# Performance work log

Hardware: AMD Instinct MI355X
Metric: run time of the kernel (lower is better)

Reference implementation:

```python
import jax, jax.numpy as jnp
import numpy as np

D_MODEL, N_HEADS, N_GROUPS, BASE = 2048, 32, 8, 10000
HEAD_DIM = D_MODEL // N_HEADS  # 64


def _rope_cache(seq, head_dim, base=BASE):
    half = head_dim // 2
    theta = 1.0 / (base ** (jnp.arange(0, head_dim, 2)[:half].astype(jnp.float32) / head_dim))
    ang = jnp.einsum('i,j->ij', jnp.arange(seq, dtype=jnp.float32), theta)  # (seq, half)
    return jnp.cos(ang), jnp.sin(ang)


def _apply_rope(x):
    # x: (b, s, h, head_dim) -> interleaved-pair rotation, matching torch module
    b, s, h, hd = x.shape
    cos, sin = _rope_cache(s, hd)
    xr = x.reshape(b, s, h, hd // 2, 2)
    c = cos[None, :, None, :]
    sn = sin[None, :, None, :]
    x0, x1 = xr[..., 0], xr[..., 1]
    out = jnp.stack((x0 * c - x1 * sn, x1 * c + x0 * sn), axis=-1)
    return out.reshape(b, s, h, hd).astype(x.dtype)


def setup_inputs() -> dict:
    key = jax.random.key(0)
    ks = jax.random.split(key, 8)
    B, S = 1, 2048
    kv_dim = HEAD_DIM * N_GROUPS
    return {
        'Q': jax.random.normal(ks[0], (B, S, D_MODEL), jnp.float32),
        'K': jax.random.normal(ks[1], (B, S, D_MODEL), jnp.float32),
        'V': jax.random.normal(ks[2], (B, S, D_MODEL), jnp.float32),
        'attention_mask': jnp.ones((B, S), jnp.int32),
        'Wq': jax.random.normal(ks[3], (D_MODEL, D_MODEL), jnp.float32) * 0.02,
        'Wk': jax.random.normal(ks[4], (D_MODEL, kv_dim), jnp.float32) * 0.02,
        'Wv': jax.random.normal(ks[5], (D_MODEL, kv_dim), jnp.float32) * 0.02,
        'Wo': jax.random.normal(ks[6], (D_MODEL, D_MODEL), jnp.float32) * 0.02,
        'bo': jnp.zeros((D_MODEL,), jnp.float32),
    }


def reference(Q, K, V, attention_mask, Wq, Wk, Wv, Wo, bo):
    b, s, _ = Q.shape
    g, hpg, hd = N_GROUPS, N_HEADS // N_GROUPS, HEAD_DIM
    # projections (weights stored as [in, out], equivalent to torch x @ W.T)
    q = (Q @ Wq).reshape(b, s, N_HEADS, hd)
    q = _apply_rope(q).reshape(b, s, g, hpg, hd)
    k = _apply_rope((K @ Wk).reshape(b, s, g, hd))
    v = (V @ Wv).reshape(b, s, g, hd)

    scale = jnp.sqrt(jnp.float32(hd))
    scores = jnp.einsum('bnghd,bmgd->bnghm', q, k) / scale  # (b, s, g, hpg, s)
    # padding mask (b, 1, 1, 1, s) and causal mask (1, s, 1, 1, s)
    pad = (attention_mask != 0)[:, None, None, None, :]
    causal = jnp.tril(jnp.ones((s, s), bool))[None, :, None, None, :]
    scores = jnp.where(pad & causal, scores, -jnp.inf)
    attn = jax.nn.softmax(scores, axis=-1)  # dropout p=0.0 -> identity
    out = jnp.einsum('bnghm,bmgd->bnghd', attn, v).reshape(b, s, D_MODEL)
    return out @ Wo + bo
```

## Files before the change

### kernel.cpp

```cpp
#include <hip/hip_runtime.h>

typedef __bf16 bf16_t;
typedef __bf16 bf16x8 __attribute__((ext_vector_type(8)));
typedef __bf16 bf16x4 __attribute__((ext_vector_type(4)));
typedef __bf16 bf16x2 __attribute__((ext_vector_type(2)));
typedef float  f32x4  __attribute__((ext_vector_type(4)));

#define LOG2E 1.44269504088896340736f

#define GLDS(gp, lp)                                                           \
  __builtin_amdgcn_global_load_lds(                                            \
      (const __attribute__((address_space(1))) void*)(gp),                     \
      (__attribute__((address_space(3))) void*)(lp), 16, 0, 0)

__global__ __launch_bounds__(256) void rope_table_k(float* __restrict__ cs,
                                                    float* __restrict__ sn, int S) {
  int i = blockIdx.x * 256 + threadIdx.x;
  if (i >= S * 32) return;
  int s = i >> 5, j = i & 31;
  float theta = powf(10000.0f, -(float)j * (1.0f / 32.0f));
  float a = (float)s * theta;
  cs[i] = cosf(a);
  sn[i] = sinf(a);
}

__global__ void transpose4_k(const float* __restrict__ Wq, const float* __restrict__ Wk,
                             const float* __restrict__ Wv, const float* __restrict__ Wo,
                             bf16_t* __restrict__ WqT, bf16_t* __restrict__ WkT,
                             bf16_t* __restrict__ WvT, bf16_t* __restrict__ WoT) {
  __shared__ float tile[32][33];
  const int bx = blockIdx.x;
  const float* in; bf16_t* out; int C, cbl;
  if (bx < 64)      { in = Wq; out = WqT; C = 2048; cbl = bx; }
  else if (bx < 80) { in = Wk; out = WkT; C = 512;  cbl = bx - 64; }
  else if (bx < 96) { in = Wv; out = WvT; C = 512;  cbl = bx - 80; }
  else              { in = Wo; out = WoT; C = 2048; cbl = bx - 96; }
  const int R = 2048;
  int c0 = cbl * 32, r0 = blockIdx.y * 32;
  int tx = threadIdx.x, ty = threadIdx.y;
  #pragma unroll
  for (int k = 0; k < 32; k += 8)
    tile[ty + k][tx] = in[(size_t)(r0 + ty + k) * C + c0 + tx];
  __syncthreads();
  #pragma unroll
  for (int k = 0; k < 32; k += 8)
    out[(size_t)(c0 + ty + k) * R + r0 + tx] = (bf16_t)tile[tx][ty + k];
}

__device__ __forceinline__ int xcd_swz(int bid, int nb) {
  const int q = nb >> 3;
  return (bid & 7) * q + (bid >> 3);
}
__device__ __forceinline__ void st_map(int lin, int nstc, int& rb, int& cb) {
  const int stid = lin >> 4, w = lin & 15;
  const int sr = stid / nstc, t = stid - sr * nstc;
  const int sc = (sr & 1) ? (nstc - 1 - t) : t;
  rb = sr * 4 + (w >> 2);
  cb = sc * 4 + (w & 3);
}

template<int MODE>
__global__ __launch_bounds__(256) void gemm_glds_k(
    const void* __restrict__ Aq, const void* __restrict__ Ak, const void* __restrict__ Av,
    const bf16_t* __restrict__ Bq, const bf16_t* __restrict__ Bk, const bf16_t* __restrict__ Bv,
    const int K, const float* __restrict__ cs, const float* __restrict__ sn,
    bf16_t* __restrict__ oq, bf16_t* __restrict__ okg, bf16_t* __restrict__ ovt,
    float* __restrict__ ofp, const float* __restrict__ bias, const int S) {
  constexpr int BN   = (MODE == 0) ? 128 : 64;
  constexpr int NI   = BN / 32;
  constexpr int BU   = BN / 32;
  constexpr int NB   = (MODE == 0) ? 768 : 1024;
  constexpr int NSTC = (MODE == 0) ? 6 : 8;
  __shared__ bf16_t a_lds[64 * 64];
  __shared__ bf16_t b_lds[BN * 64];
  const int tid = threadIdx.x, wid = tid >> 6, lane = tid & 63;
  const int fr = lane & 15, kg = lane >> 4;

  const int lin = xcd_swz(blockIdx.x, NB);
  int rb, cb; st_map(lin, NSTC, rb, cb);
  const void* Ap; const bf16_t* Bp; int emode, col0;
  if (MODE == 1)    { Ap = Aq; Bp = Bq; emode = 3; col0 = cb * BN; }
  else if (cb < 16) { Ap = Aq; Bp = Bq; emode = 0; col0 = cb * 128; }
  else if (cb < 20) { Ap = Ak; Bp = Bk; emode = 1; col0 = (cb - 16) * 128; }
  else              { Ap = Av; Bp = Bv; emode = 2; col0 = (cb - 20) * 128; }
  const int row0 = rb * 64;
  const int wr = (wid >> 1) * 32, wc = (wid & 1) * (BN / 2);

  f32x4 acc[2][NI];
  #pragma unroll
  for (int i = 0; i < 2; ++i)
    #pragma unroll
    for (int j = 0; j < NI; ++j)
      acc[i][j] = (f32x4){0.f, 0.f, 0.f, 0.f};

  const int rloc = lane >> 3;
  const int schunk = ((lane & 7) ^ rloc) * 8;
  const bf16_t* gB[BU];
  bf16_t* lB[BU];
  #pragma unroll
  for (int u = 0; u < BU; ++u) {
    gB[u] = Bp + (size_t)(col0 + (wid * BU + u) * 8 + rloc) * K + schunk;
    lB[u] = &b_lds[(wid * BU + u) * 512];
  }

#define MFMA_STEP                                                              \
  do {                                                                         \
    _Pragma("unroll")                                                          \
    for (int ks = 0; ks < 2; ++ks) {                                           \
      bf16x8 af[2], bfr[NI];                                                   \
      _Pragma("unroll")                                                        \
      for (int mi = 0; mi < 2; ++mi) {                                         \
        const int r = wr + mi * 16 + fr;                                       \
        af[mi] = *(const bf16x8*)&a_lds[r * 64 + (((ks * 4 + kg) ^ (fr & 7)) * 8)]; \
      }                                                                        \
      _Pragma("unroll")                                                        \
      for (int ni = 0; ni < NI; ++ni) {                                        \
        const int r = wc + ni * 16 + fr;                                       \
        bfr[ni] = *(const bf16x8*)&b_lds[r * 64 + (((ks * 4 + kg) ^ (fr & 7)) * 8)]; \
      }                                                                        \
      _Pragma("unroll")                                                        \
      for (int mi = 0; mi < 2; ++mi)                                           \
        _Pragma("unroll")                                                      \
        for (int ni = 0; ni < NI; ++ni)                                        \
          acc[mi][ni] = __builtin_amdgcn_mfma_f32_16x16x32_bf16(af[mi], bfr[ni], acc[mi][ni], 0, 0, 0); \
    }                                                                          \
  } while (0)

  if (MODE == 0) {
    const float* Afp = (const float*)Ap;
    const int arow = wid * 16 + (lane >> 2);
    const int acol = (lane & 3) * 16;
    const int c0w = (lane & 3) * 2;
    const int wofs0 = arow * 64 + ((c0w ^ (arow & 7)) * 8);
    const int wofs1 = arow * 64 + (((c0w + 1) ^ (arow & 7)) * 8);
    const float* abase = &Afp[(size_t)(row0 + arow) * K + acol];
    f32x4 pA0, pA1, pA2, pA3, pB0, pB1, pB2, pB3;
    pA0 = *(const f32x4*)(abase);      pA1 = *(const f32x4*)(abase + 4);
    pA2 = *(const f32x4*)(abase + 8);  pA3 = *(const f32x4*)(abase + 12);
    pB0 = *(const f32x4*)(abase + 64); pB1 = *(const f32x4*)(abase + 68);
    pB2 = *(const f32x4*)(abase + 72); pB3 = *(const f32x4*)(abase + 76);

#define A_WRITE(r0_, r1_, r2_, r3_)                                            \
    do {                                                                       \
      bf16x8 w0, w1;                                                           \
      w0[0]=(bf16_t)r0_[0]; w0[1]=(bf16_t)r0_[1]; w0[2]=(bf16_t)r0_[2]; w0[3]=(bf16_t)r0_[3]; \
      w0[4]=(bf16_t)r1_[0]; w0[5]=(bf16_t)r1_[1]; w0[6]=(bf16_t)r1_[2]; w0[7]=(bf16_t)r1_[3]; \
      w1[0]=(bf16_t)r2_[0]; w1[1]=(bf16_t)r2_[1]; w1[2]=(bf16_t)r2_[2]; w1[3]=(bf16_t)r2_[3]; \
      w1[4]=(bf16_t)r3_[0]; w1[5]=(bf16_t)r3_[1]; w1[6]=(bf16_t)r3_[2]; w1[7]=(bf16_t)r3_[3]; \
      *(bf16x8*)&a_lds[wofs0] = w0;                                            \
      *(bf16x8*)&a_lds[wofs1] = w1;                                            \
    } while (0)

    for (int kt = 0; kt < K; kt += 128) {
      __syncthreads();
      A_WRITE(pA0, pA1, pA2, pA3);
      #pragma unroll
      for (int u = 0; u < BU; ++u) GLDS(gB[u] + kt, lB[u]);
      __syncthreads();
      if (kt + 128 < K) {
        const float* p = abase + kt + 128;
        pA0 = *(const f32x4*)(p);     pA1 = *(const f32x4*)(p + 4);
        pA2 = *(const f32x4*)(p + 8); pA3 = *(const f32x4*)(p + 12);
      }
      MFMA_STEP;
      __syncthreads();
      A_WRITE(pB0, pB1, pB2, pB3);
      #pragma unroll
      for (int u = 0; u < BU; ++u) GLDS(gB[u] + kt + 64, lB[u]);
      __syncthreads();
      if (kt + 192 < K) {
        const float* p = abase + kt + 192;
        pB0 = *(const f32x4*)(p);     pB1 = *(const f32x4*)(p + 4);
        pB2 = *(const f32x4*)(p + 8); pB3 = *(const f32x4*)(p + 12);
      }
      MFMA_STEP;
    }
#undef A_WRITE
  } else {
    const bf16_t* gA0 = (const bf16_t*)Ap + (size_t)(row0 + (wid * 2 + 0) * 8 + rloc) * K + schunk;
    const bf16_t* gA1 = (const bf16_t*)Ap + (size_t)(row0 + (wid * 2 + 1) * 8 + rloc) * K + schunk;
    bf16_t* lA0 = &a_lds[(wid * 2 + 0) * 512];
    bf16_t* lA1 = &a_lds[(wid * 2 + 1) * 512];
    for (int kt = 0; kt < K; kt += 64) {
      __syncthreads();
      GLDS(gA0 + kt, lA0);
      GLDS(gA1 + kt, lA1);
      #pragma unroll
      for (int u = 0; u < BU; ++u) GLDS(gB[u] + kt, lB[u]);
      __syncthreads();
      MFMA_STEP;
    }
  }
#undef MFMA_STEP

  #pragma unroll
  for (int mi = 0; mi < 2; ++mi) {
    #pragma unroll
    for (int ni = 0; ni < NI; ++ni) {
      #pragma unroll
      for (int r = 0; r < 4; ++r) {
        const int grow = row0 + wr + mi * 16 + kg * 4 + r;
        const int gcol = col0 + wc + ni * 16 + fr;
        float v = acc[mi][ni][r];
        if (emode == 3) {
          ofp[(size_t)grow * 2048 + gcol] = v + bias[gcol];
        } else if (emode == 2) {
          const int gi = gcol >> 6, d = gcol & 63;
          ovt[((size_t)gi * 64 + d) * S + grow] = (bf16_t)v;
        } else {
          const float pv = __shfl_xor(v, 1);
          const int d = gcol & 63, p = d >> 1, hh = gcol >> 6;
          const float c = cs[grow * 32 + p], s = sn[grow * 32 + p];
          float o = (d & 1) ? fmaf(pv, s, v * c) : fmaf(-pv, s, v * c);
          if (emode == 0) {
            o *= 0.125f * LOG2E;
            oq[((size_t)hh * S + grow) * 64 + d] = (bf16_t)o;
          } else {
            okg[((size_t)hh * S + grow) * 64 + d] = (bf16_t)o;
          }
        }
      }
    }
  }
}

__device__ __forceinline__ int swz8(int r, int c) { return r * 64 + (((c) ^ (r & 7)) << 3); }

__global__ __launch_bounds__(256) void attn_k(
    const bf16_t* __restrict__ qh,
    const bf16_t* __restrict__ kgr,
    const bf16_t* __restrict__ vtg,
    const int* __restrict__ amask,
    bf16_t* __restrict__ ao,
    const int S) {
  __shared__ bf16_t k_lds[64 * 64];
  __shared__ bf16_t vt_lds[64 * 64];
  __shared__ bf16_t p_lds[4][16 * 64];
  const int tid = threadIdx.x, wid = tid >> 6, lane = tid & 63;
  const int fr = lane & 15, kgp = lane >> 4;
  const int h = blockIdx.x, g = h >> 2;
  const int qb = 31 - blockIdx.y;
  const int q0 = qb * 64 + wid * 16;
  const int qg = q0 + fr;

  const bf16_t* qbase = qh + ((size_t)h * S + q0 + fr) * 64;
  const bf16x8 qf0 = *(const bf16x8*)&qbase[kgp * 8];
  const bf16x8 qf1 = *(const bf16x8*)&qbase[32 + kgp * 8];

  f32x4 oacc[4];
  #pragma unroll
  for (int t = 0; t < 4; ++t) oacc[t] = (f32x4){0.f, 0.f, 0.f, 0.f};
  float m_ = -1e30f, l_ = 0.f;

  const int srow = tid >> 2, sc4 = tid & 3;
  const bf16_t* kbase = kgr + (size_t)g * S * 64;
  const bf16_t* vbase = vtg + (size_t)g * 64 * S;
  const int cmax = qb + 1;

  bf16x8 nk0 = *(const bf16x8*)&kbase[(size_t)srow * 64 + sc4 * 8];
  bf16x8 nk1 = *(const bf16x8*)&kbase[(size_t)srow * 64 + 32 + sc4 * 8];
  bf16x8 nv0 = *(const bf16x8*)&vbase[(size_t)srow * S + sc4 * 8];
  bf16x8 nv1 = *(const bf16x8*)&vbase[(size_t)srow * S + 32 + sc4 * 8];
  int mvc = amask[lane];
  *(bf16x8*)&k_lds[swz8(srow, sc4)]      = nk0;
  *(bf16x8*)&k_lds[swz8(srow, 4 + sc4)]  = nk1;
  *(bf16x8*)&vt_lds[swz8(srow, sc4)]     = nv0;
  *(bf16x8*)&vt_lds[swz8(srow, 4 + sc4)] = nv1;
  __syncthreads();

  for (int c = 0; c < cmax; ++c) {
    const int kc0 = c * 64;
    const unsigned long long pm = __ballot(mvc == 0);
    const bool more = (c + 1 < cmax);
    if (more) {
      const int kc1 = kc0 + 64;
      nk0 = *(const bf16x8*)&kbase[(size_t)(kc1 + srow) * 64 + sc4 * 8];
      nk1 = *(const bf16x8*)&kbase[(size_t)(kc1 + srow) * 64 + 32 + sc4 * 8];
      nv0 = *(const bf16x8*)&vbase[(size_t)srow * S + kc1 + sc4 * 8];
      nv1 = *(const bf16x8*)&vbase[(size_t)srow * S + kc1 + 32 + sc4 * 8];
      mvc = amask[kc1 + lane];
    }

    f32x4 sc[4];
    #pragma unroll
    for (int a = 0; a < 4; ++a) {
      const bf16x8 ka0 = *(const bf16x8*)&k_lds[swz8(a * 16 + fr, kgp)];
      const bf16x8 ka1 = *(const bf16x8*)&k_lds[swz8(a * 16 + fr, 4 + kgp)];
      f32x4 z = (f32x4){0.f, 0.f, 0.f, 0.f};
      z = __builtin_amdgcn_mfma_f32_16x16x32_bf16(ka0, qf0, z, 0, 0, 0);
      z = __builtin_amdgcn_mfma_f32_16x16x32_bf16(ka1, qf1, z, 0, 0, 0);
      sc[a] = z;
    }

    if (c == qb) {
      #pragma unroll
      for (int a = 0; a < 4; ++a)
        #pragma unroll
        for (int r = 0; r < 4; ++r) {
          const int kl = a * 16 + 4 * kgp + r;
          if (kc0 + kl > qg) sc[a][r] = -1e30f;
        }
    }
    if (pm) {
      #pragma unroll
      for (int a = 0; a < 4; ++a)
        #pragma unroll
        for (int r = 0; r < 4; ++r) {
          const int kl = a * 16 + 4 * kgp + r;
          if ((pm >> kl) & 1) sc[a][r] = -1e30f;
        }
    }

    float t0 = fmaxf(fmaxf(sc[0][0], sc[0][1]), fmaxf(sc[0][2], sc[0][3]));
    float t1 = fmaxf(fmaxf(sc[1][0], sc[1][1]), fmaxf(sc[1][2], sc[1][3]));
    float t2 = fmaxf(fmaxf(sc[2][0], sc[2][1]), fmaxf(sc[2][2], sc[2][3]));
    float t3 = fmaxf(fmaxf(sc[3][0], sc[3][1]), fmaxf(sc[3][2], sc[3][3]));
    float smax = fmaxf(fmaxf(t0, t1), fmaxf(t2, t3));
    smax = fmaxf(smax, __shfl_xor(smax, 16));
    smax = fmaxf(smax, __shfl_xor(smax, 32));

    const bool rescale = !__all(smax <= m_ + 8.0f);
    if (rescale) {
      const float mn = fmaxf(m_, smax);
      const float al = exp2f(m_ - mn);
      m_ = mn;
      #pragma unroll
      for (int t = 0; t < 4; ++t)
        #pragma unroll
        for (int r = 0; r < 4; ++r) oacc[t][r] *= al;
      l_ *= al;
    }

    float ps = 0.f;
    #pragma unroll
    for (int a = 0; a < 4; ++a)
      #pragma unroll
      for (int r = 0; r < 4; ++r) {
        const float p = exp2f(sc[a][r] - m_);
        sc[a][r] = p;
        ps += p;
      }
    ps += __shfl_xor(ps, 16);
    ps += __shfl_xor(ps, 32);
    l_ += ps;

    #pragma unroll
    for (int a = 0; a < 4; ++a) {
      bf16x4 w;
      w[0] = (bf16_t)sc[a][0];
      w[1] = (bf16_t)sc[a][1];
      w[2] = (bf16_t)sc[a][2];
      w[3] = (bf16_t)sc[a][3];
      const int off = a * 16 + 4 * kgp;
      *(bf16x4*)&p_lds[wid][fr * 64 + (((off >> 3) ^ (fr & 7)) << 3) + (off & 7)] = w;
    }
    const bf16x8 pa0 = *(const bf16x8*)&p_lds[wid][swz8(fr, kgp)];
    const bf16x8 pa1 = *(const bf16x8*)&p_lds[wid][swz8(fr, 4 + kgp)];

    #pragma unroll
    for (int t = 0; t < 4; ++t) {
      const bf16x8 vb0 = *(const bf16x8*)&vt_lds[swz8(t * 16 + fr, kgp)];
      const bf16x8 vb1 = *(const bf16x8*)&vt_lds[swz8(t * 16 + fr, 4 + kgp)];
      oacc[t] = __builtin_amdgcn_mfma_f32_16x16x32_bf16(vb0, pa0, oacc[t], 0, 0, 0);
      oacc[t] = __builtin_amdgcn_mfma_f32_16x16x32_bf16(vb1, pa1, oacc[t], 0, 0, 0);
    }

    if (more) {
      __syncthreads();
      *(bf16x8*)&k_lds[swz8(srow, sc4)]      = nk0;
      *(bf16x8*)&k_lds[swz8(srow, 4 + sc4)]  = nk1;
      *(bf16x8*)&vt_lds[swz8(srow, sc4)]     = nv0;
      *(bf16x8*)&vt_lds[swz8(srow, 4 + sc4)] = nv1;
      __syncthreads();
    }
  }

  const float inv = 1.0f / l_;
  #pragma unroll
  for (int t = 0; t < 4; ++t) {
    bf16x4 o4;
    #pragma unroll
    for (int r = 0; r < 4; ++r) o4[r] = (bf16_t)(oacc[t][r] * inv);
    *(bf16x4*)&ao[(size_t)(q0 + fr) * 2048 + h * 64 + t * 16 + 4 * kgp] = o4;
  }
}

extern "C" void kernel_launch(void* const* d_in, const int* in_sizes, int n_in,
                              void* d_out, int out_size, void* d_ws, size_t ws_size,
                              hipStream_t stream) {
  const float* Q  = (const float*)d_in[0];
  const float* K  = (const float*)d_in[1];
  const float* V  = (const float*)d_in[2];
  const int*   am = (const int*)d_in[3];
  const float* Wq = (const float*)d_in[4];
  const float* Wk = (const float*)d_in[5];
  const float* Wv = (const float*)d_in[6];
  const float* Wo = (const float*)d_in[7];
  const float* bo = (const float*)d_in[8];
  float* out = (float*)d_out;

  const int S = 2048, D = 2048;
  char* w = (char*)d_ws;
  const size_t MB = 1u << 20;
  bf16_t* WqT = (bf16_t*)(w + 0 * MB);
  bf16_t* WoT = (bf16_t*)(w + 8 * MB);
  bf16_t* WkT = (bf16_t*)(w + 16 * MB);
  bf16_t* WvT = (bf16_t*)(w + 18 * MB);
  bf16_t* qh  = (bf16_t*)(w + 20 * MB);
  bf16_t* kgr = (bf16_t*)(w + 28 * MB);
  bf16_t* vtg = (bf16_t*)(w + 30 * MB);
  bf16_t* ao  = (bf16_t*)(w + 32 * MB);
  float*  cs  = (float*)(w + 40 * MB);
  float*  sn  = (float*)(w + 40 * MB + 256 * 1024);

  rope_table_k<<<256, 256, 0, stream>>>(cs, sn, S);
  transpose4_k<<<dim3(160, 64), dim3(32, 8), 0, stream>>>(Wq, Wk, Wv, Wo, WqT, WkT, WvT, WoT);

  gemm_glds_k<0><<<768, 256, 0, stream>>>(Q, K, V, WqT, WkT, WvT, D,
                                          cs, sn, qh, kgr, vtg, nullptr, nullptr, S);

  attn_k<<<dim3(32, 32), 256, 0, stream>>>(qh, kgr, vtg, am, ao, S);

  gemm_glds_k<1><<<1024, 256, 0, stream>>>(ao, nullptr, nullptr, WoT, nullptr, nullptr,
                                           D, nullptr, nullptr, nullptr, nullptr, nullptr,
                                           out, bo, S);
}
```

Before: 142.0 us.

## Double-buffer LDS tiles in projection GEMMs to overlap loads with MFMA

Gives the A and B shared-memory tiles two buffers in both GEMM modes. Each iteration stages the next K-slice into the alternate buffer while MFMAs run on the current one, with a single barrier per iteration instead of two. This is meant to hide global-to-LDS latency and cut synchronization stalls. The cost is twice the LDS per block, which may lower occupancy.

Measured after the change: 147.3 us. +3.7%, slower.

```diff
diff --git a/kernel.cpp b/kernel.cpp
--- a/kernel.cpp
+++ b/kernel.cpp
@@ -71,8 +71,8 @@
   constexpr int BU   = BN / 32;
   constexpr int NB   = (MODE == 0) ? 768 : 1024;
   constexpr int NSTC = (MODE == 0) ? 6 : 8;
-  __shared__ bf16_t a_lds[64 * 64];
-  __shared__ bf16_t b_lds[BN * 64];
+  __shared__ bf16_t a_lds[2][64 * 64];
+  __shared__ bf16_t b_lds[2][BN * 64];
   const int tid = threadIdx.x, wid = tid >> 6, lane = tid & 63;
   const int fr = lane & 15, kg = lane >> 4;
 
@@ -96,14 +96,18 @@
   const int rloc = lane >> 3;
   const int schunk = ((lane & 7) ^ rloc) * 8;
   const bf16_t* gB[BU];
-  bf16_t* lB[BU];
-  #pragma unroll
-  for (int u = 0; u < BU; ++u) {
+  #pragma unroll
+  for (int u = 0; u < BU; ++u)
     gB[u] = Bp + (size_t)(col0 + (wid * BU + u) * 8 + rloc) * K + schunk;
-    lB[u] = &b_lds[(wid * BU + u) * 512];
-  }
-
-#define MFMA_STEP                                                              \
+  const int lBo = (wid * BU) * 512;
+
+#define STAGE_B(buf, kt)                                                       \
+  do {                                                                         \
+    _Pragma("unroll")                                                          \
+    for (int u = 0; u < BU; ++u) GLDS(gB[u] + (kt), &b_lds[buf][lBo + u * 512]); \
+  } while (0)
+
+#define MFMA_STEP(buf)                                                         \
   do {                                                                         \
     _Pragma("unroll")                                                          \
     for (int ks = 0; ks < 2; ++ks) {                                           \
@@ -111,12 +115,12 @@
       _Pragma("unroll")                                                        \
       for (int mi = 0; mi < 2; ++mi) {                                         \
         const int r = wr + mi * 16 + fr;                                       \
-        af[mi] = *(const bf16x8*)&a_lds[r * 64 + (((ks * 4 + kg) ^ (fr & 7)) * 8)]; \
+        af[mi] = *(const bf16x8*)&a_lds[buf][r * 64 + (((ks * 4 + kg) ^ (fr & 7)) * 8)]; \
       }                                                                        \
       _Pragma("unroll")                                                        \
       for (int ni = 0; ni < NI; ++ni) {                                        \
         const int r = wc + ni * 16 + fr;                                       \
-        bfr[ni] = *(const bf16x8*)&b_lds[r * 64 + (((ks * 4 + kg) ^ (fr & 7)) * 8)]; \
+        bfr[ni] = *(const bf16x8*)&b_lds[buf][r * 64 + (((ks * 4 + kg) ^ (fr & 7)) * 8)]; \
       }                                                                        \
       _Pragma("unroll")                                                        \
       for (int mi = 0; mi < 2; ++mi)                                           \
@@ -134,64 +138,74 @@
     const int wofs0 = arow * 64 + ((c0w ^ (arow & 7)) * 8);
     const int wofs1 = arow * 64 + (((c0w + 1) ^ (arow & 7)) * 8);
     const float* abase = &Afp[(size_t)(row0 + arow) * K + acol];
-    f32x4 pA0, pA1, pA2, pA3, pB0, pB1, pB2, pB3;
-    pA0 = *(const f32x4*)(abase);      pA1 = *(const f32x4*)(abase + 4);
-    pA2 = *(const f32x4*)(abase + 8);  pA3 = *(const f32x4*)(abase + 12);
-    pB0 = *(const f32x4*)(abase + 64); pB1 = *(const f32x4*)(abase + 68);
-    pB2 = *(const f32x4*)(abase + 72); pB3 = *(const f32x4*)(abase + 76);
-
-#define A_WRITE(r0_, r1_, r2_, r3_)                                            \
+    f32x4 r0_, r1_, r2_, r3_;
+
+#define LOAD_A(off)                                                            \
+    do {                                                                       \
+      const float* p = abase + (off);                                          \
+      r0_ = *(const f32x4*)(p);     r1_ = *(const f32x4*)(p + 4);              \
+      r2_ = *(const f32x4*)(p + 8); r3_ = *(const f32x4*)(p + 12);             \
+    } while (0)
+#define A_WRITE(buf)                                                           \
     do {                                                                       \
       bf16x8 w0, w1;                                                           \
       w0[0]=(bf16_t)r0_[0]; w0[1]=(bf16_t)r0_[1]; w0[2]=(bf16_t)r0_[2]; w0[3]=(bf16_t)r0_[3]; \
       w0[4]=(bf16_t)r1_[0]; w0[5]=(bf16_t)r1_[1]; w0[6]=(bf16_t)r1_[2]; w0[7]=(bf16_t)r1_[3]; \
       w1[0]=(bf16_t)r2_[0]; w1[1]=(bf16_t)r2_[1]; w1[2]=(bf16_t)r2_[2]; w1[3]=(bf16_t)r2_[3]; \
       w1[4]=(bf16_t)r3_[0]; w1[5]=(bf16_t)r3_[1]; w1[6]=(bf16_t)r3_[2]; w1[7]=(bf16_t)r3_[3]; \
-      *(bf16x8*)&a_lds[wofs0] = w0;                                            \
-      *(bf16x8*)&a_lds[wofs1] = w1;                                            \
+      *(bf16x8*)&a_lds[buf][wofs0] = w0;                                       \
+      *(bf16x8*)&a_lds[buf][wofs1] = w1;                                       \
     } while (0)
 
-    for (int kt = 0; kt < K; kt += 128) {
-      __syncthreads();
-      A_WRITE(pA0, pA1, pA2, pA3);
-      #pragma unroll
-      for (int u = 0; u < BU; ++u) GLDS(gB[u] + kt, lB[u]);
-      __syncthreads();
-      if (kt + 128 < K) {
-        const float* p = abase + kt + 128;
-        pA0 = *(const f32x4*)(p);     pA1 = *(const f32x4*)(p + 4);
-        pA2 = *(const f32x4*)(p + 8); pA3 = *(const f32x4*)(p + 12);
-      }
-      MFMA_STEP;
-      __syncthreads();
-      A_WRITE(pB0, pB1, pB2, pB3);
-      #pragma unroll
-      for (int u = 0; u < BU; ++u) GLDS(gB[u] + kt + 64, lB[u]);
-      __syncthreads();
-      if (kt + 192 < K) {
-        const float* p = abase + kt + 192;
-        pB0 = *(const f32x4*)(p);     pB1 = *(const f32x4*)(p + 4);
-        pB2 = *(const f32x4*)(p + 8); pB3 = *(const f32x4*)(p + 12);
-      }
-      MFMA_STEP;
-    }
+    LOAD_A(0);
+    A_WRITE(0);
+    STAGE_B(0, 0);
+    LOAD_A(64);
+    __syncthreads();
+
+    int cur = 0;
+    for (int kt = 0; kt < K; kt += 64) {
+      const bool more = (kt + 64 < K);
+      if (more) {
+        A_WRITE(cur ^ 1);
+        STAGE_B(cur ^ 1, kt + 64);
+        if (kt + 128 < K) LOAD_A(kt + 128);
+      }
+      MFMA_STEP(cur);
+      if (more) {
+        __syncthreads();
+        cur ^= 1;
+      }
+    }
+#undef LOAD_A
 #undef A_WRITE
   } else {
     const bf16_t* gA0 = (const bf16_t*)Ap + (size_t)(row0 + (wid * 2 + 0) * 8 + rloc) * K + schunk;
     const bf16_t* gA1 = (const bf16_t*)Ap + (size_t)(row0 + (wid * 2 + 1) * 8 + rloc) * K + schunk;
-    bf16_t* lA0 = &a_lds[(wid * 2 + 0) * 512];
-    bf16_t* lA1 = &a_lds[(wid * 2 + 1) * 512];
+    const int lAo0 = (wid * 2 + 0) * 512, lAo1 = (wid * 2 + 1) * 512;
+
+    GLDS(gA0, &a_lds[0][lAo0]);
+    GLDS(gA1, &a_lds[0][lAo1]);
+    STAGE_B(0, 0);
+    __syncthreads();
+
+    int cur = 0;
     for (int kt = 0; kt < K; kt += 64) {
-      __syncthreads();
-      GLDS(gA0 + kt, lA0);
-      GLDS(gA1 + kt, lA1);
-      #pragma unroll
-      for (int u = 0; u < BU; ++u) GLDS(gB[u] + kt, lB[u]);
-      __syncthreads();
-      MFMA_STEP;
+      const bool more = (kt + 64 < K);
+      if (more) {
+        GLDS(gA0 + kt + 64, &a_lds[cur ^ 1][lAo0]);
+        GLDS(gA1 + kt + 64, &a_lds[cur ^ 1][lAo1]);
+        STAGE_B(cur ^ 1, kt + 64);
+      }
+      MFMA_STEP(cur);
+      if (more) {
+        __syncthreads();
+        cur ^= 1;
+      }
     }
   }
 #undef MFMA_STEP
+#undef STAGE_B
 
   #pragma unroll
   for (int mi = 0; mi < 2; ++mi) {
```
